# Performance work log

Hardware: AMD Instinct MI355X
Metric: run time of the kernel (lower is better)

The kernel has to match this reference:

```python
import jax, jax.numpy as jnp
import numpy as np

B, NUMS, SEQ, H, LAYERS, PRED = 128, 128, 256, 1024, 2, 96


def setup_inputs() -> dict:
    key = jax.random.key(0)
    ks = jax.random.split(key, 7)
    s = 0.02
    return {
        "x": jax.random.normal(ks[0], (B, NUMS, SEQ), jnp.float32),
        "W0": jax.random.normal(ks[1], (NUMS + H, 4 * H), jnp.float32) * s,
        "b0": jax.random.normal(ks[2], (4 * H,), jnp.float32) * s,
        "W1": jax.random.normal(ks[3], (H + H, 4 * H), jnp.float32) * s,
        "b1": jax.random.normal(ks[4], (4 * H,), jnp.float32) * s,
        "fc_w": jax.random.normal(ks[5], (H, PRED), jnp.float32) * s,
        "fc_b": jax.random.normal(ks[6], (PRED,), jnp.float32) * s,
    }


def _lstm_layer(x_seq, W, b, h0, c0):
    # x_seq: [B, T, D]; W packs the four gate linears [D+H, 4H] (i,f,o,g)
    def step(carry, xt):
        h, c = carry
        z = jnp.concatenate([xt, h], axis=1) @ W + b  # [B, 4H]
        i, f, o, g = jnp.split(z, 4, axis=1)
        i, f, o = jax.nn.sigmoid(i), jax.nn.sigmoid(f), jax.nn.sigmoid(o)
        c = f * c + i * jnp.tanh(g)
        h = o * jnp.tanh(c)
        return (h, c), h

    (h, c), hs = jax.lax.scan(step, (h0, c0), jnp.swapaxes(x_seq, 0, 1))
    return jnp.swapaxes(hs, 0, 1), h, c  # [B, T, H], [B, H], [B, H]


def reference(x, W0, b0, W1, b1, fc_w, fc_b):
    bsz = x.shape[0]
    h = jnp.zeros((bsz, H), x.dtype)
    c = jnp.zeros((bsz, H), x.dtype)
    seq = jnp.swapaxes(x, 1, 2)  # [B, T, NUMS]
    # NB: faithful to source, (h, c) carry over across layers (no reset)
    seq, h, c = _lstm_layer(seq, W0, b0, h, c)
    seq, h, c = _lstm_layer(seq, W1, b1, h, c)
    out = jnp.tanh(seq[:, -1, :] @ fc_w + fc_b)  # [B, PRED]
    return (out, h, c)
```

## Files before the change

### kernel.cpp

```cpp
#include <hip/hip_runtime.h>
#include <stdint.h>

#define Bsz  128
#define NUMS 128
#define SEQn 256
#define Hn   1024
#define PRED 96
#define G4H  4096
#define GN   256
#define BH   ((size_t)Bsz*Hn)

typedef __attribute__((ext_vector_type(8))) short bf16x8;
typedef __attribute__((ext_vector_type(4))) float f32x4;

template<int N> struct IC { static constexpr int value = N; };

__device__ __forceinline__ unsigned short f2bf(float x){
  union { float f; unsigned u; } v; v.f = x;
  return (unsigned short)((v.u + 0x7FFFu + ((v.u >> 16) & 1u)) >> 16);
}
__device__ __forceinline__ float fast_tanh(float x){
  return 1.f - 2.f/(1.f + __expf(2.f*x));
}

__global__ void pack_x_kernel(const float* __restrict__ x, unsigned short* __restrict__ xp){
  __shared__ float tile[64][65];
  const int t0 = blockIdx.x * 64, n0 = blockIdx.y * 64, b = blockIdx.z;
  const int tid = threadIdx.x;
  const int c = tid & 63, r = tid >> 6;
  #pragma unroll
  for (int i = 0; i < 16; i++){
    int n = r + i*4;
    tile[n][c] = x[((size_t)b*NUMS + n0 + n)*SEQn + t0 + c];
  }
  __syncthreads();
  #pragma unroll
  for (int i = 0; i < 16; i++){
    int t = r + i*4;
    xp[((size_t)(t0+t)*Bsz + b)*NUMS + n0 + c] = f2bf(tile[c][t]);
  }
}

__global__ void pack_w_kernel(const float* __restrict__ W, unsigned short* __restrict__ Wpk,
                              int KST, int row_off, int kstride, int kof){
  const int u = blockIdx.x * blockDim.x + threadIdx.x;
  if (u >= 256*KST*64) return;
  const int lane = u & 63;
  const int kst  = (u >> 6) % KST;
  const int cgg  = (u >> 6) / KST;
  const int nb = cgg >> 2, gate = cgg & 3;
  const int col = gate*Hn + nb*16 + (lane & 15);
  const int kbase = row_off + kst*32 + (lane >> 4)*8;
  unsigned short tmp[8];
  #pragma unroll
  for (int e = 0; e < 8; e++) tmp[e] = f2bf(W[(size_t)(kbase+e)*G4H + col]);
  ((ulonglong2*)Wpk)[(size_t)(cgg*kstride + kof + kst)*64 + lane] = *(const ulonglong2*)tmp;
}

__global__ void zero_kernel(unsigned short* __restrict__ h0, float* __restrict__ c,
                            unsigned* __restrict__ bars){
  int i = blockIdx.x*256 + threadIdx.x;
  if (i < Bsz*Hn){ h0[i] = 0; c[i] = 0.0f; }
  if (i < 2048) bars[i] = 0u;
}

template<int K1, int S2, int KTOT, int LAYER, bool RING2>
__global__ __launch_bounds__(512, 2)
void persist_kernel(const unsigned short* __restrict__ xpp,
                    unsigned short* __restrict__ hring,
                    unsigned short* __restrict__ h1b,
                    const unsigned short* __restrict__ Wpk,
                    const float* __restrict__ bias,
                    float* __restrict__ cst,
                    float* __restrict__ hf_out,
                    unsigned* __restrict__ bar)
{
  constexpr int KST_TOT = KTOT/32;
  constexpr int HALF = KST_TOT/2;
  constexpr int NCH = (KTOT + 511)/512;
  constexpr int NBUF = (LAYER == 0) ? 2 : 4;
  __shared__ unsigned short sa[NBUF][32*512];
  __shared__ unsigned short sxb[(LAYER == 0) ? 32*128 : 64];
  __shared__ float se[2][4*32*18];

  const int tid = threadIdx.x;
  const int w = tid >> 6, l = tid & 63;
  const int blk = blockIdx.x;
  const int q = blk >> 3;
  const int nb = (blk & 7)*8 + (q & 7);
  const int mb = q >> 3;
  const int ksh = w & 1, cgi = w >> 1;
  const int cgg = nb*4 + cgi;
  const int lrow = l & 15, lg = l >> 4;
  const int bgrp = blk >> 3;

  bf16x8 wreg[HALF];
  #pragma unroll
  for (int j = 0; j < HALF; j++)
    wreg[j] = *(const bf16x8*)(Wpk + ((size_t)(cgg*KST_TOT + 2*j + ksh)*64 + l)*8);

  unsigned offA[4];
  #pragma unroll
  for (int ii = 0; ii < 4; ii++){
    const int flat = ii*8 + w;
    const int kst_l = flat >> 1, mi = flat & 1;
    offA[ii] = (unsigned)((mb*32 + mi*16 + lrow)*1024 + kst_l*32 + lg*8);
  }
  const unsigned offX = (unsigned)((mb*32 + (w & 1)*16 + lrow)*S2 + (w >> 1)*32 + lg*8);

  const int erow = tid >> 4, ejj = tid & 15;
  const int R = mb*32 + erow;
  const int J = nb*16 + ejj;
  const size_t idx = (size_t)R*Hn + J;
  float creg = (LAYER == 0) ? 0.f : cst[idx];

  auto stageF = [&](auto CHC, const unsigned short* tilebase){
    constexpr int ch = decltype(CHC)::value;
    constexpr bool coh = (LAYER == 1 && !RING2 && ch >= 2);
    const unsigned short* b2 = tilebase + (ch & 1)*512;
    #pragma unroll
    for (int ii = 0; ii < 4; ii++){
      const unsigned short* src = b2 + offA[ii];
      if constexpr (coh)
        __builtin_amdgcn_global_load_lds(
          (const __attribute__((address_space(1))) void*)src,
          (__attribute__((address_space(3))) void*)&sa[ch][(ii*8 + w)*512], 16, 0, 17);
      else
        __builtin_amdgcn_global_load_lds(
          (const __attribute__((address_space(1))) void*)src,
          (__attribute__((address_space(3))) void*)&sa[ch][(ii*8 + w)*512], 16, 0, 0);
    }
  };
  auto stageX = [&](const unsigned short* xbase){
    __builtin_amdgcn_global_load_lds(
      (const __attribute__((address_space(1))) void*)(xbase + offX),
      (__attribute__((address_space(3))) void*)&sxb[w*512], 16, 0, 0);
  };

  for (int t = 0; t < SEQn; ++t){
    #pragma unroll
    for (int j = 0; j < HALF; j++) asm volatile("" : "+v"(wreg[j]));

    const unsigned short* A1;
    const unsigned short* A2;
    unsigned short* hout;
    if (LAYER == 0){
      A1   = hring + (size_t)t*BH;
      A2   = xpp + (size_t)t*Bsz*NUMS;
      hout = hring + (size_t)(t+1)*BH;
    } else {
      A1   = hring + (size_t)(t+1)*BH;
      A2   = (t == 0) ? (hring + (size_t)SEQn*BH)
                      : (h1b + (size_t)(RING2 ? (t-1) : ((t-1)&1))*BH);
      hout = h1b + (size_t)(RING2 ? t : (t&1))*BH;
    }

    f32x4 acc2[2] = {{0.f,0.f,0.f,0.f},{0.f,0.f,0.f,0.f}};

    auto comp = [&](auto CHC){
      constexpr int ch = decltype(CHC)::value;
      if constexpr (ch < NCH){
        constexpr bool isx = (LAYER == 0 && ch == NCH-1);
        constexpr int nksl = isx ? 2 : 8;
        const unsigned short* ab = isx ? sxb : sa[ch];
        #pragma unroll
        for (int ksl = 0; ksl < nksl; ksl++){
          const int klocal = ksl*2 + ksh;
          const int wj = isx ? (16 + ksl) : (ch*8 + ksl);
          bf16x8 af0 = *(const bf16x8*)&ab[((klocal*2 + 0)*64 + l)*8];
          bf16x8 af1 = *(const bf16x8*)&ab[((klocal*2 + 1)*64 + l)*8];
          acc2[0] = __builtin_amdgcn_mfma_f32_16x16x32_bf16(af0, wreg[wj], acc2[0], 0, 0, 0);
          acc2[1] = __builtin_amdgcn_mfma_f32_16x16x32_bf16(af1, wreg[wj], acc2[1], 0, 0, 0);
        }
      }
    };

    if (t == 0){
      stageF(IC<0>{}, A1); stageF(IC<1>{}, A1);
      if constexpr (LAYER == 1){ stageF(IC<2>{}, A2); stageF(IC<3>{}, A2); }
      else                       stageX(A2);
      __syncthreads();
      comp(IC<0>{}); comp(IC<1>{}); comp(IC<2>{}); comp(IC<3>{});
    } else if constexpr (LAYER == 1){
      stageF(IC<2>{}, A2); stageF(IC<3>{}, A2);
      comp(IC<0>{}); comp(IC<1>{});
      __syncthreads();
      comp(IC<2>{}); comp(IC<3>{});
    } else {
      stageF(IC<0>{}, A1); stageF(IC<1>{}, A1);
      comp(IC<2>{});
      __syncthreads();
      comp(IC<0>{}); comp(IC<1>{});
    }

    {
      #pragma unroll
      for (int mi = 0; mi < 2; mi++)
        #pragma unroll
        for (int r = 0; r < 4; r++){
          const int row2 = mi*16 + lg*4 + r;
          se[ksh][(cgi*32 + row2)*18 + lrow] = acc2[mi][r];
        }
    }
    __syncthreads();
    {
      float zi = se[0][(0*32+erow)*18 + ejj] + se[1][(0*32+erow)*18 + ejj];
      float zf = se[0][(1*32+erow)*18 + ejj] + se[1][(1*32+erow)*18 + ejj];
      float zo = se[0][(2*32+erow)*18 + ejj] + se[1][(2*32+erow)*18 + ejj];
      float zg = se[0][(3*32+erow)*18 + ejj] + se[1][(3*32+erow)*18 + ejj];
      zi += bias[0*Hn + J]; zf += bias[1*Hn + J];
      zo += bias[2*Hn + J]; zg += bias[3*Hn + J];
      const float gi = 1.f/(1.f + __expf(-zi));
      const float gf = 1.f/(1.f + __expf(-zf));
      const float go = 1.f/(1.f + __expf(-zo));
      const float gg = fast_tanh(zg);
      creg = gf * creg + gi * gg;
      const float hn = go * fast_tanh(creg);
      const unsigned hu   = (unsigned)f2bf(hn);
      const unsigned mate = (unsigned)__shfl_xor((int)hu, 1);
      if ((l & 1) == 0){
        const unsigned pk = hu | (mate << 16);
        __hip_atomic_store((unsigned*)(hout + idx), pk,
                           __ATOMIC_RELAXED, __HIP_MEMORY_SCOPE_AGENT);
      }
      if (t == SEQn-1){
        cst[idx] = creg;
        if (LAYER == 1) hf_out[idx] = hn;
      }
    }

    if (t + 1 < SEQn){
      __syncthreads();
      if (tid == 0){
        const unsigned ga = __hip_atomic_fetch_add(&bar[bgrp*16], 1u,
                              __ATOMIC_RELAXED, __HIP_MEMORY_SCOPE_AGENT);
        if (ga == (unsigned)(t*8 + 7)){
          const unsigned ra = __hip_atomic_fetch_add(&bar[512], 1u,
                                __ATOMIC_RELAXED, __HIP_MEMORY_SCOPE_AGENT);
          if (ra == (unsigned)(t*32 + 31))
            __hip_atomic_store(&bar[528], (unsigned)(t+1),
                               __ATOMIC_RELAXED, __HIP_MEMORY_SCOPE_AGENT);
        }
      }
      if constexpr (LAYER == 1){
        const unsigned short* A1n = hring + (size_t)(t+2)*BH;
        stageF(IC<0>{}, A1n);
        stageF(IC<1>{}, A1n);
      } else {
        stageX(xpp + (size_t)(t+1)*Bsz*NUMS);
      }
      if (tid == 0){
        while (__hip_atomic_load(&bar[528], __ATOMIC_RELAXED,
                                 __HIP_MEMORY_SCOPE_AGENT) < (unsigned)(t+1))
          __builtin_amdgcn_s_sleep(1);
      }
      __syncthreads();
    }
  }
}

__global__ __launch_bounds__(256)
void fc_out_kernel(const float* __restrict__ hf, const float* __restrict__ cst,
                   const float* __restrict__ fcw, const float* __restrict__ fcb,
                   float* __restrict__ dout){
  __shared__ float hrow[Hn];
  const int b = blockIdx.x, tid = threadIdx.x;
  for (int i = tid; i < Hn; i += 256) hrow[i] = hf[(size_t)b*Hn + i];
  __syncthreads();
  if (tid < PRED){
    float a = fcb[tid];
    for (int k = 0; k < Hn; k++) a += hrow[k] * fcw[(size_t)k*PRED + tid];
    dout[(size_t)b*PRED + tid] = tanhf(a);
  }
  for (int i = tid; i < Hn; i += 256){
    dout[Bsz*PRED + (size_t)b*Hn + i] = hf[(size_t)b*Hn + i];
    dout[Bsz*PRED + (size_t)Bsz*Hn + (size_t)b*Hn + i] = cst[(size_t)b*Hn + i];
  }
}

extern "C" void kernel_launch(void* const* d_in, const int* in_sizes, int n_in,
                              void* d_out, int out_size, void* d_ws, size_t ws_size,
                              hipStream_t stream){
  const float* x   = (const float*)d_in[0];
  const float* W0  = (const float*)d_in[1];
  const float* b0  = (const float*)d_in[2];
  const float* W1  = (const float*)d_in[3];
  const float* b1  = (const float*)d_in[4];
  const float* fcw = (const float*)d_in[5];
  const float* fcb = (const float*)d_in[6];
  float* dout = (float*)d_out;

  char* p = (char*)d_ws;
  auto alloc = [&](size_t bytes)->void*{
    void* r = (void*)p; p += (bytes + 255) & ~(size_t)255; return r;
  };
  unsigned short* xp   = (unsigned short*)alloc((size_t)SEQn*Bsz*NUMS*2);
  unsigned short* Wpk0 = (unsigned short*)alloc((size_t)256*36*64*8*2);
  unsigned short* Wpk1 = (unsigned short*)alloc((size_t)256*64*64*8*2);
  unsigned short* H0   = (unsigned short*)alloc((size_t)(SEQn+1)*BH*2);
  float* cst = (float*)alloc((size_t)BH*4);
  float* hf  = (float*)alloc((size_t)BH*4);
  unsigned* bars = (unsigned*)alloc((size_t)2048*sizeof(unsigned));

  const bool big = ws_size >= (size_t)176*1024*1024;
  unsigned short* h1b;
  if (big) h1b = (unsigned short*)alloc((size_t)SEQn*BH*2);
  else     h1b = (unsigned short*)alloc((size_t)2*BH*2);

  pack_x_kernel<<<dim3(SEQn/64, NUMS/64, Bsz), dim3(256), 0, stream>>>(x, xp);
  pack_w_kernel<<<dim3((256*32*64 + 255)/256), dim3(256), 0, stream>>>(W0, Wpk0, 32, 128, 36, 0);
  pack_w_kernel<<<dim3((256*4*64  + 255)/256), dim3(256), 0, stream>>>(W0, Wpk0,  4,   0, 36, 32);
  pack_w_kernel<<<dim3((256*64*64 + 255)/256), dim3(256), 0, stream>>>(W1, Wpk1, 64, 0, 64, 0);
  zero_kernel<<<dim3((Bsz*Hn + 255)/256), dim3(256), 0, stream>>>(H0, cst, bars);

  persist_kernel<1024, NUMS, 1152, 0, false><<<dim3(GN), dim3(512), 0, stream>>>(
      xp, H0, nullptr, Wpk0, b0, cst, nullptr, bars);

  if (big){
    persist_kernel<1024, Hn, 2048, 1, true><<<dim3(GN), dim3(512), 0, stream>>>(
        nullptr, H0, h1b, Wpk1, b1, cst, hf, bars + 1024);
  } else {
    persist_kernel<1024, Hn, 2048, 1, false><<<dim3(GN), dim3(512), 0, stream>>>(
        nullptr, H0, h1b, Wpk1, b1, cst, hf, bars + 1024);
  }

  fc_out_kernel<<<dim3(Bsz), dim3(256), 0, stream>>>(hf, cst, fcw, fcb, dout);
}
```

Measured before the change: 3.373 ms.

## Replace global grid barrier with per-row-block half-column counters polled before staging

Drops the hierarchical grid-wide barrier (group counter, root counter, release flag) that ran every timestep. Each block now bumps a counter for its batch-row block and column half. Before staging each half of the recurrent input, the block polls only the counter covering the producers of that half. Prefetch of the next step's independent operand (x tile or layer-0 h) moves earlier, ahead of the gate math. This narrows the dependency to the blocks that actually produce the data and lets staging of the first half overlap with producers of the second half. The cost is that every thread polls, and correctness now depends on the counter indexing matching the block-to-tile mapping, with no acquire ordering on the relaxed atomics.

```diff
diff --git a/kernel.cpp b/kernel.cpp
--- a/kernel.cpp
+++ b/kernel.cpp
@@ -92,7 +92,8 @@
   const int ksh = w & 1, cgi = w >> 1;
   const int cgg = nb*4 + cgi;
   const int lrow = l & 15, lg = l >> 4;
-  const int bgrp = blk >> 3;
+  const int myhalf = nb >> 5;
+  unsigned* mycnt = bar + mb*64;
 
   bf16x8 wreg[HALF];
   #pragma unroll
@@ -135,6 +136,11 @@
     __builtin_amdgcn_global_load_lds(
       (const __attribute__((address_space(1))) void*)(xbase + offX),
       (__attribute__((address_space(3))) void*)&sxb[w*512], 16, 0, 0);
+  };
+  auto pollHalf = [&](int half, unsigned target){
+    const unsigned* cw = mycnt + half*16;
+    while (__hip_atomic_load(cw, __ATOMIC_RELAXED, __HIP_MEMORY_SCOPE_AGENT) < target)
+      __builtin_amdgcn_s_sleep(1);
   };
 
   for (int t = 0; t < SEQn; ++t){
@@ -182,12 +188,14 @@
       __syncthreads();
       comp(IC<0>{}); comp(IC<1>{}); comp(IC<2>{}); comp(IC<3>{});
     } else if constexpr (LAYER == 1){
-      stageF(IC<2>{}, A2); stageF(IC<3>{}, A2);
+      pollHalf(0, 32u*(unsigned)t); stageF(IC<2>{}, A2);
+      pollHalf(1, 32u*(unsigned)t); stageF(IC<3>{}, A2);
       comp(IC<0>{}); comp(IC<1>{});
       __syncthreads();
       comp(IC<2>{}); comp(IC<3>{});
     } else {
-      stageF(IC<0>{}, A1); stageF(IC<1>{}, A1);
+      pollHalf(0, 32u*(unsigned)t); stageF(IC<0>{}, A1);
+      pollHalf(1, 32u*(unsigned)t); stageF(IC<1>{}, A1);
       comp(IC<2>{});
       __syncthreads();
       comp(IC<0>{}); comp(IC<1>{});
@@ -203,6 +211,17 @@
         }
     }
     __syncthreads();
+
+    if (t + 1 < SEQn){
+      if constexpr (LAYER == 1){
+        const unsigned short* A1n = hring + (size_t)(t+2)*BH;
+        stageF(IC<0>{}, A1n);
+        stageF(IC<1>{}, A1n);
+      } else {
+        stageX(xpp + (size_t)(t+1)*Bsz*NUMS);
+      }
+    }
+
     {
       float zi = se[0][(0*32+erow)*18 + ejj] + se[1][(0*32+erow)*18 + ejj];
       float zf = se[0][(1*32+erow)*18 + ejj] + se[1][(1*32+erow)*18 + ejj];
@@ -231,30 +250,9 @@
 
     if (t + 1 < SEQn){
       __syncthreads();
-      if (tid == 0){
-        const unsigned ga = __hip_atomic_fetch_add(&bar[bgrp*16], 1u,
-                              __ATOMIC_RELAXED, __HIP_MEMORY_SCOPE_AGENT);
-        if (ga == (unsigned)(t*8 + 7)){
-          const unsigned ra = __hip_atomic_fetch_add(&bar[512], 1u,
-                                __ATOMIC_RELAXED, __HIP_MEMORY_SCOPE_AGENT);
-          if (ra == (unsigned)(t*32 + 31))
-            __hip_atomic_store(&bar[528], (unsigned)(t+1),
+      if (tid == 0)
+        __hip_atomic_fetch_add(mycnt + myhalf*16, 1u,
                                __ATOMIC_RELAXED, __HIP_MEMORY_SCOPE_AGENT);
-        }
-      }
-      if constexpr (LAYER == 1){
-        const unsigned short* A1n = hring + (size_t)(t+2)*BH;
-        stageF(IC<0>{}, A1n);
-        stageF(IC<1>{}, A1n);
-      } else {
-        stageX(xpp + (size_t)(t+1)*Bsz*NUMS);
-      }
-      if (tid == 0){
-        while (__hip_atomic_load(&bar[528], __ATOMIC_RELAXED,
-                                 __HIP_MEMORY_SCOPE_AGENT) < (unsigned)(t+1))
-          __builtin_amdgcn_s_sleep(1);
-      }
-      __syncthreads();
     }
   }
 }
```

Measured after the change: 2.850 ms. 15.5% less time.
